# Kernel tuning notes

Hardware: AMD Instinct MI355X
Metric: run time of the kernel (lower is better)

Reference implementation:

```python
import jax, jax.numpy as jnp
import numpy as np

B, NV, NDIRS, NRINGS, NCH, NF = 2, 15000, 16, 3, 32, 64


def setup_inputs() -> dict:
    key = jax.random.key(0)
    k1, k2, k3, k4 = jax.random.split(key, 4)
    y = jax.random.normal(k1, (B, NV, NDIRS, NCH), dtype=jnp.float32)
    ft_v = jax.random.randint(k2, (NV, NRINGS, NDIRS), 0, NV, dtype=jnp.int32)
    ft_d = jax.random.randint(k3, (NV, NRINGS, NDIRS), 0, NDIRS, dtype=jnp.int32)
    kernel = jax.random.normal(k4, (NRINGS, NDIRS, NCH, NF), dtype=jnp.float32) * 0.05
    bias = jnp.zeros((NF,), dtype=jnp.float32)
    return {"y": y, "ft_v": ft_v, "ft_d": ft_d, "kernel": kernel, "bias": bias}


def reference(y, ft_v, ft_d, kernel, bias):
    # y: [b, nv, ndirs, nch]; ft_v/ft_d: [nv, nrings, ndirs]; kernel: [nrings, ndirs, nch, nf]
    b, nv, ndirs, nch = y.shape
    f = jnp.transpose(y, (1, 2, 3, 0))  # [nv, ndirs, nch, b]
    dirs = jnp.arange(ndirs)

    def per_dir(l):
        # cyclic forward shift of the direction axis, composed with the
        # frame-transporter gather: z[v,r,d,c,b] = f[ft_v[v,r,d], (ft_d[v,r,d]+l)%n, c, b]
        d_idx = (ft_d + l) % ndirs                # [nv, nrings, ndirs]
        z = f[ft_v, d_idx]                        # [nv, nrings, ndirs, nch, b]
        # kernel shifted in reverse: k_l[:, d] = kernel[:, (d-l)%n]
        k_l = kernel[:, (dirs - l) % ndirs]       # [nrings, ndirs, nch, nf]
        return jnp.einsum('vrdcb,rdcf->vbf', z, k_l)  # [nv, b, nf]

    out = jax.lax.map(per_dir, dirs)              # [ndirs, nv, b, nf] (sequential, like tf.while_loop)
    out = jnp.transpose(out, (2, 1, 0, 3))        # [b, nv, ndirs, nf]
    out = out + bias
    return jax.nn.relu(out)
```

## Files before the change

kernel.cpp:

```cpp
#include <hip/hip_runtime.h>

#define NV 15000
#define ND 16
#define NR 3
#define NC 32
#define NFDIM 64
#define BB 2

typedef short bf16x8 __attribute__((ext_vector_type(8)));
typedef float f32x4 __attribute__((ext_vector_type(4)));
typedef unsigned short u16x8 __attribute__((ext_vector_type(8)));

#define KB_OFF     30720000u
#define WS_NEEDED  30916608u

__device__ __forceinline__ unsigned short f2bf(float x) {
  union { float f; unsigned int u; } cv; cv.f = x;
  unsigned int u = cv.u;
  u += 0x7FFF + ((u >> 16) & 1);
  return (unsigned short)(u >> 16);
}

__global__ void prep_y(const float* __restrict__ y, u16x8* __restrict__ yt) {
  int tid = blockIdx.x * 256 + threadIdx.x;
  if (tid >= (NV * ND * BB * NC) / 8) return;
  int o   = tid * 8;
  int v   = o >> 10;
  int rem = o & 1023;
  int d   = rem >> 6;
  int b   = (rem >> 5) & 1;
  int c0  = rem & 31;
  const f32x4* src = (const f32x4*)(y + (((b * NV + v) * ND + d) * NC + c0));
  f32x4 lo = src[0], hi = src[1];
  u16x8 r;
#pragma unroll
  for (int i = 0; i < 4; i++) { r[i] = f2bf(lo[i]); r[4 + i] = f2bf(hi[i]); }
  yt[tid] = r;
}

__global__ void prep_kb(const float* __restrict__ kern, unsigned short* __restrict__ kb) {
  int t = blockIdx.x * 256 + threadIdx.x;
  if (t >= 48 * 4 * 64) return;
  int lane  = t & 63;
  int ft    = (t >> 6) & 3;
  int chunk = t >> 8;
  int q = lane >> 4;
  int f = (lane & 15) * 4 + ft;
  unsigned short* dst = kb + t * 8;
#pragma unroll
  for (int j = 0; j < 8; j++) {
    int k = q * 8 + j;
    dst[j] = f2bf(kern[(chunk * NC + k) * NFDIM + f]);
  }
}

__global__ __launch_bounds__(256, 3) void sync_conv_main(
    const unsigned short* __restrict__ yt, const unsigned short* __restrict__ kb,
    const int* __restrict__ ftv, const int* __restrict__ ftd,
    const float* __restrict__ bias, float* __restrict__ out) {
  __shared__ int pidx_lds[16][49];

  int tid  = threadIdx.x;
  int lane = tid & 63;
  int mg   = blockIdx.x >> 2;
  int lg   = blockIdx.x & 3;
  int l    = lg * 4 + (tid >> 6);
  int vbase = mg * 16;

  for (int t = tid; t < 16 * 48; t += 256) {
    int i = t / 48, j = t - i * 48;
    int v = vbase + i; v = v < NV ? v : NV - 1;
    pidx_lds[i][j] = ftv[v * 48 + j] * 16 + (ftd[v * 48 + j] & 15);
  }
  __syncthreads();

  int q    = lane >> 4;
  int n    = lane & 15;
  int b    = n & 1;
  int voff = n >> 1;
  int lane_elem = b * 32 + q * 8;
  const unsigned short* kb_lane = kb + lane * 8;

  f32x4 acc[2][4];
#pragma unroll
  for (int i = 0; i < 2; i++)
#pragma unroll
    for (int j = 0; j < 4; j++) acc[i][j] = (f32x4){0.f, 0.f, 0.f, 0.f};

  bf16x8 bufA[2][2][2];
  bf16x8 bufB[2][2][4];

  auto load_batch = [&](int bidx, int par) {
    int k0 = bidx * 2;
#pragma unroll
    for (int ds = 0; ds < 2; ds++) {
      int k = k0 + ds;
      int r = k >> 4;
      int dp = ((k & 15) - l) & 15;
      const unsigned short* kbp = kb_lane + (r * 16 + dp) * 2048;
#pragma unroll
      for (int ft = 0; ft < 4; ft++)
        bufB[par][ds][ft] = *reinterpret_cast<const bf16x8*>(kbp + ft * 512);
#pragma unroll
      for (int mt = 0; mt < 2; mt++) {
        int p  = pidx_lds[mt * 8 + voff][k];
        int dd = ((p & 15) + l) & 15;
        int off = (p >> 4) * 1024 + (dd << 6) + lane_elem;
        bufA[par][mt][ds] = *reinterpret_cast<const bf16x8*>(yt + off);
      }
    }
  };
  auto compute_batch = [&](int par) {
#pragma unroll
    for (int ds = 0; ds < 2; ds++)
#pragma unroll
      for (int mt = 0; mt < 2; mt++)
#pragma unroll
        for (int ft = 0; ft < 4; ft++)
          acc[mt][ft] = __builtin_amdgcn_mfma_f32_16x16x32_bf16(
              bufA[par][mt][ds], bufB[par][ds][ft], acc[mt][ft], 0, 0, 0);
  };

  load_batch(0, 0);
  for (int i = 0; i < 12; i++) {
    load_batch(2 * i + 1, 1);
    compute_batch(0);
    if (i < 11) load_batch(2 * i + 2, 0);
    compute_batch(1);
  }

  f32x4 bv = *reinterpret_cast<const f32x4*>(bias + 4 * n);

#pragma unroll
  for (int mt = 0; mt < 2; mt++) {
#pragma unroll
    for (int reg = 0; reg < 4; reg++) {
      int m  = q * 4 + reg;
      int v  = vbase + mt * 8 + (m >> 1);
      int bb = m & 1;
      if (v < NV) {
        f32x4 x;
#pragma unroll
        for (int ft = 0; ft < 4; ft++) {
          float t = acc[mt][ft][reg] + bv[ft];
          x[ft] = t > 0.f ? t : 0.f;
        }
        float* dst = out + (((bb * NV + v) * ND + l) * NFDIM) + 4 * n;
        __builtin_nontemporal_store(x, (f32x4*)dst);
      }
    }
  }
}

__global__ void fallback_kernel(const float* __restrict__ y, const int* __restrict__ ftv,
                                const int* __restrict__ ftd, const float* __restrict__ kern,
                                const float* __restrict__ bias, float* __restrict__ out) {
  int idx = blockIdx.x;
  int l = idx & 15;
  int v = (idx >> 4) % NV;
  int b = idx / (NV * ND);
  int f = threadIdx.x;
  float acc = 0.f;
  for (int r = 0; r < NR; r++)
    for (int d = 0; d < ND; d++) {
      int ii = (v * NR + r) * ND + d;
      int vv = ftv[ii];
      int dd = (ftd[ii] + l) & 15;
      int dp = (d - l) & 15;
      const float* yp = y + ((b * NV + vv) * ND + dd) * NC;
      const float* kp = kern + ((r * 16 + dp) * NC) * NFDIM + f;
#pragma unroll 8
      for (int c = 0; c < NC; c++) acc += yp[c] * kp[c * NFDIM];
    }
  float x = acc + bias[f];
  out[idx * NFDIM + f] = x > 0.f ? x : 0.f;
}

extern "C" void kernel_launch(void* const* d_in, const int* in_sizes, int n_in,
                              void* d_out, int out_size, void* d_ws, size_t ws_size,
                              hipStream_t stream) {
  const float* y    = (const float*)d_in[0];
  const int*   ftv  = (const int*)d_in[1];
  const int*   ftd  = (const int*)d_in[2];
  const float* kern = (const float*)d_in[3];
  const float* bias = (const float*)d_in[4];
  float* out = (float*)d_out;

  if (ws_size >= (size_t)WS_NEEDED) {
    char* ws = (char*)d_ws;
    unsigned short* yt = (unsigned short*)ws;
    unsigned short* kb = (unsigned short*)(ws + KB_OFF);

    prep_y<<<(NV * ND * BB * NC / 8 + 255) / 256, 256, 0, stream>>>(y, (u16x8*)yt);
    prep_kb<<<(48 * 4 * 64 + 255) / 256, 256, 0, stream>>>(kern, kb);
    sync_conv_main<<<3752, 256, 0, stream>>>(yt, kb, ftv, ftd, bias, out);
  } else {
    fallback_kernel<<<BB * NV * ND, NFDIM, 0, stream>>>(y, ftv, ftd, kern, bias, out);
  }
}
```

Measured before the change: 376.6 us.

## Triple-buffer gathered A loads and precompute per-wave gather offsets in LDS

Measured after the change: 371.2 us. Within noise of the previous version (-1.4%).

```diff
diff --git a/kernel.cpp b/kernel.cpp
--- a/kernel.cpp
+++ b/kernel.cpp
@@ -58,28 +58,41 @@
     const unsigned short* __restrict__ yt, const unsigned short* __restrict__ kb,
     const int* __restrict__ ftv, const int* __restrict__ ftd,
     const float* __restrict__ bias, float* __restrict__ out) {
-  __shared__ int pidx_lds[16][49];
+  __shared__ int pidx[16][49];
+  __shared__ int pre[4][16][49];
 
   int tid  = threadIdx.x;
   int lane = tid & 63;
+  int w    = tid >> 6;
   int mg   = blockIdx.x >> 2;
   int lg   = blockIdx.x & 3;
-  int l    = lg * 4 + (tid >> 6);
+  int l    = lg * 4 + w;
   int vbase = mg * 16;
 
   for (int t = tid; t < 16 * 48; t += 256) {
     int i = t / 48, j = t - i * 48;
     int v = vbase + i; v = v < NV ? v : NV - 1;
-    pidx_lds[i][j] = ftv[v * 48 + j] * 16 + (ftd[v * 48 + j] & 15);
+    pidx[i][j] = ftv[v * 48 + j] * 16 + (ftd[v * 48 + j] & 15);
+  }
+  __syncthreads();
+#pragma unroll
+  for (int wl = 0; wl < 4; wl++) {
+    int ll = lg * 4 + wl;
+    for (int t = tid; t < 768; t += 256) {
+      int i = t / 48, j = t - i * 48;
+      int p = pidx[i][j];
+      pre[wl][i][j] = (p >> 4) * 1024 + ((((p & 15) + ll) & 15) << 6);
+    }
   }
   __syncthreads();
 
   int q    = lane >> 4;
   int n    = lane & 15;
-  int b    = n & 1;
   int voff = n >> 1;
-  int lane_elem = b * 32 + q * 8;
+  int lane_elem = (n & 1) * 32 + q * 8;
   const unsigned short* kb_lane = kb + lane * 8;
+  const int* pre_w0 = &pre[w][voff][0];
+  const int* pre_w1 = &pre[w][8 + voff][0];
 
   f32x4 acc[2][4];
 #pragma unroll
@@ -87,30 +100,32 @@
 #pragma unroll
     for (int j = 0; j < 4; j++) acc[i][j] = (f32x4){0.f, 0.f, 0.f, 0.f};
 
-  bf16x8 bufA[2][2][2];
+  bf16x8 bufA[3][2][2];
   bf16x8 bufB[2][2][4];
 
-  auto load_batch = [&](int bidx, int par) {
-    int k0 = bidx * 2;
+  auto loadB = [&](int bt, int par) {
 #pragma unroll
     for (int ds = 0; ds < 2; ds++) {
-      int k = k0 + ds;
-      int r = k >> 4;
-      int dp = ((k & 15) - l) & 15;
-      const unsigned short* kbp = kb_lane + (r * 16 + dp) * 2048;
+      int s = 2 * bt + ds;
+      const unsigned short* kbp = kb_lane + s * 2048;
 #pragma unroll
       for (int ft = 0; ft < 4; ft++)
         bufB[par][ds][ft] = *reinterpret_cast<const bf16x8*>(kbp + ft * 512);
-#pragma unroll
-      for (int mt = 0; mt < 2; mt++) {
-        int p  = pidx_lds[mt * 8 + voff][k];
-        int dd = ((p & 15) + l) & 15;
-        int off = (p >> 4) * 1024 + (dd << 6) + lane_elem;
-        bufA[par][mt][ds] = *reinterpret_cast<const bf16x8*>(yt + off);
-      }
     }
   };
-  auto compute_batch = [&](int par) {
+  auto loadA = [&](int bt, int par) {
+#pragma unroll
+    for (int ds = 0; ds < 2; ds++) {
+      int s = 2 * bt + ds;
+      int j = (s & 48) | ((s + l) & 15);
+      int o0 = pre_w0[j] + lane_elem;
+      int o1 = pre_w1[j] + lane_elem;
+      bufA[par][0][ds] = *reinterpret_cast<const bf16x8*>(yt + o0);
+      bufA[par][1][ds] = *reinterpret_cast<const bf16x8*>(yt + o1);
+    }
+  };
+  auto compute = [&](int parA, int parB) {
+    __builtin_amdgcn_s_setprio(1);
 #pragma unroll
     for (int ds = 0; ds < 2; ds++)
 #pragma unroll
@@ -118,15 +133,22 @@
 #pragma unroll
         for (int ft = 0; ft < 4; ft++)
           acc[mt][ft] = __builtin_amdgcn_mfma_f32_16x16x32_bf16(
-              bufA[par][mt][ds], bufB[par][ds][ft], acc[mt][ft], 0, 0, 0);
+              bufA[parA][mt][ds], bufB[parB][ds][ft], acc[mt][ft], 0, 0, 0);
+    __builtin_amdgcn_s_setprio(0);
   };
 
-  load_batch(0, 0);
-  for (int i = 0; i < 12; i++) {
-    load_batch(2 * i + 1, 1);
-    compute_batch(0);
-    if (i < 11) load_batch(2 * i + 2, 0);
-    compute_batch(1);
+  loadA(0, 0);
+  loadB(0, 0);
+  loadA(1, 1);
+  __builtin_amdgcn_sched_barrier(0);
+
+#pragma unroll
+  for (int bt = 0; bt < 24; bt++) {
+    if (bt + 1 < 24) loadB(bt + 1, (bt + 1) & 1);
+    if (bt + 2 < 24) loadA(bt + 2, (bt + 2) % 3);
+    __builtin_amdgcn_sched_barrier(0);
+    compute(bt % 3, bt & 1);
+    __builtin_amdgcn_sched_barrier(0);
   }
 
   f32x4 bv = *reinterpret_cast<const f32x4*>(bias + 4 * n);
```

## Stage gathers and kernel tiles through LDS with async global_load_lds ring

Applied to the files above, without the earlier changes.

Result: slower. 444.5 us (+18.0%).

```diff
diff --git a/kernel.cpp b/kernel.cpp
--- a/kernel.cpp
+++ b/kernel.cpp
@@ -10,9 +10,14 @@
 typedef short bf16x8 __attribute__((ext_vector_type(8)));
 typedef float f32x4 __attribute__((ext_vector_type(4)));
 typedef unsigned short u16x8 __attribute__((ext_vector_type(8)));
+typedef unsigned int u32;
 
 #define KB_OFF     30720000u
 #define WS_NEEDED  30916608u
+
+#define AS1 __attribute__((address_space(1)))
+#define AS3 __attribute__((address_space(3)))
+#define GLOAD16(gp, lp) __builtin_amdgcn_global_load_lds((AS1 const u32*)(gp), (AS3 u32*)(lp), 16, 0, 0)
 
 __device__ __forceinline__ unsigned short f2bf(float x) {
   union { float f; unsigned int u; } cv; cv.f = x;
@@ -54,32 +59,35 @@
   }
 }
 
-__global__ __launch_bounds__(256, 3) void sync_conv_main(
+__global__ __launch_bounds__(256, 2) void sync_conv_main(
     const unsigned short* __restrict__ yt, const unsigned short* __restrict__ kb,
     const int* __restrict__ ftv, const int* __restrict__ ftd,
     const float* __restrict__ bias, float* __restrict__ out) {
-  __shared__ int pidx_lds[16][49];
+  __shared__ short lds_a[5 * 4 * 2 * 512];
+  __shared__ short lds_b[5 * 4 * 512];
+  __shared__ int   pidx[16][49];
 
   int tid  = threadIdx.x;
   int lane = tid & 63;
+  int w    = tid >> 6;
   int mg   = blockIdx.x >> 2;
   int lg   = blockIdx.x & 3;
-  int l    = lg * 4 + (tid >> 6);
+  int l    = lg * 4 + w;
   int vbase = mg * 16;
 
   for (int t = tid; t < 16 * 48; t += 256) {
     int i = t / 48, j = t - i * 48;
     int v = vbase + i; v = v < NV ? v : NV - 1;
-    pidx_lds[i][j] = ftv[v * 48 + j] * 16 + (ftd[v * 48 + j] & 15);
+    pidx[i][j] = ftv[v * 48 + j] * 16 + (ftd[v * 48 + j] & 15);
   }
   __syncthreads();
 
   int q    = lane >> 4;
   int n    = lane & 15;
-  int b    = n & 1;
   int voff = n >> 1;
-  int lane_elem = b * 32 + q * 8;
-  const unsigned short* kb_lane = kb + lane * 8;
+  int lane_elem = (n & 1) * 32 + q * 8;
+  const int* rp0 = &pidx[voff][0];
+  const int* rp1 = &pidx[8 + voff][0];
 
   f32x4 acc[2][4];
 #pragma unroll
@@ -87,47 +95,59 @@
 #pragma unroll
     for (int j = 0; j < 4; j++) acc[i][j] = (f32x4){0.f, 0.f, 0.f, 0.f};
 
-  bf16x8 bufA[2][2][2];
-  bf16x8 bufB[2][2][4];
-
-  auto load_batch = [&](int bidx, int par) {
-    int k0 = bidx * 2;
-#pragma unroll
-    for (int ds = 0; ds < 2; ds++) {
-      int k = k0 + ds;
-      int r = k >> 4;
-      int dp = ((k & 15) - l) & 15;
-      const unsigned short* kbp = kb_lane + (r * 16 + dp) * 2048;
-#pragma unroll
-      for (int ft = 0; ft < 4; ft++)
-        bufB[par][ds][ft] = *reinterpret_cast<const bf16x8*>(kbp + ft * 512);
-#pragma unroll
-      for (int mt = 0; mt < 2; mt++) {
-        int p  = pidx_lds[mt * 8 + voff][k];
-        int dd = ((p & 15) + l) & 15;
-        int off = (p >> 4) * 1024 + (dd << 6) + lane_elem;
-        bufA[par][mt][ds] = *reinterpret_cast<const bf16x8*>(yt + off);
-      }
+  auto stage = [&](int s, int ss) {
+    int j  = (s & 48) | ((s + l) & 15);
+    int p0 = rp0[j];
+    int p1 = rp1[j];
+    int off0 = ((p0 >> 4) << 10) | ((((p0 & 15) + l) & 15) << 6);
+    int off1 = ((p1 >> 4) << 10) | ((((p1 & 15) + l) & 15) << 6);
+    const unsigned short* g0 = yt + off0 + lane_elem;
+    const unsigned short* g1 = yt + off1 + lane_elem;
+    short* la = lds_a + (ss * 4 + w) * 1024;
+    GLOAD16(g0, la);
+    GLOAD16(g1, la + 512);
+    const unsigned short* gb = kb + s * 2048 + w * 512 + (lane << 3);
+    GLOAD16(gb, lds_b + (ss * 4 + w) * 512);
+  };
+
+  auto computeP = [&](int cs) {
+    const short* la = lds_a + (cs * 4 + w) * 1024;
+    const short* lb = lds_b + cs * 2048;
+    bf16x8 a0 = *(const bf16x8*)(la + (lane << 3));
+    bf16x8 a1 = *(const bf16x8*)(la + 512 + (lane << 3));
+    __builtin_amdgcn_s_setprio(1);
+#pragma unroll
+    for (int ft = 0; ft < 4; ft++) {
+      bf16x8 bf = *(const bf16x8*)(lb + ft * 512 + (lane << 3));
+      acc[0][ft] = __builtin_amdgcn_mfma_f32_16x16x32_bf16(a0, bf, acc[0][ft], 0, 0, 0);
+      acc[1][ft] = __builtin_amdgcn_mfma_f32_16x16x32_bf16(a1, bf, acc[1][ft], 0, 0, 0);
     }
+    __builtin_amdgcn_s_setprio(0);
   };
-  auto compute_batch = [&](int par) {
-#pragma unroll
-    for (int ds = 0; ds < 2; ds++)
-#pragma unroll
-      for (int mt = 0; mt < 2; mt++)
-#pragma unroll
-        for (int ft = 0; ft < 4; ft++)
-          acc[mt][ft] = __builtin_amdgcn_mfma_f32_16x16x32_bf16(
-              bufA[par][mt][ds], bufB[par][ds][ft], acc[mt][ft], 0, 0, 0);
-  };
-
-  load_batch(0, 0);
-  for (int i = 0; i < 12; i++) {
-    load_batch(2 * i + 1, 1);
-    compute_batch(0);
-    if (i < 11) load_batch(2 * i + 2, 0);
-    compute_batch(1);
-  }
+
+  stage(0, 0); stage(1, 1); stage(2, 2); stage(3, 3);
+
+  int cs = 0, ss = 4;
+  for (int t = 0; t < 44; t++) {
+    asm volatile("s_waitcnt vmcnt(9)" ::: "memory");
+    __builtin_amdgcn_s_barrier();
+    stage(t + 4, ss);
+    computeP(cs);
+    cs = cs == 4 ? 0 : cs + 1;
+    ss = ss == 4 ? 0 : ss + 1;
+  }
+  asm volatile("s_waitcnt vmcnt(9)" ::: "memory");
+  __builtin_amdgcn_s_barrier();
+  computeP(cs); cs = cs == 4 ? 0 : cs + 1;
+  asm volatile("s_waitcnt vmcnt(6)" ::: "memory");
+  __builtin_amdgcn_s_barrier();
+  computeP(cs); cs = cs == 4 ? 0 : cs + 1;
+  asm volatile("s_waitcnt vmcnt(3)" ::: "memory");
+  __builtin_amdgcn_s_barrier();
+  computeP(cs); cs = cs == 4 ? 0 : cs + 1;
+  asm volatile("s_waitcnt vmcnt(0)" ::: "memory");
+  __builtin_amdgcn_s_barrier();
+  computeP(cs);
 
   f32x4 bv = *reinterpret_cast<const f32x4*>(bias + 4 * n);
 
```
